# Performance work log

Measured on AMD Instinct MI355X. Metric: run time of the kernel, lower is better.

## Reference

```python
import jax, jax.numpy as jnp
import numpy as np

N = 10000      # n_nodes
T = 8          # input_horizon
P = 2          # prediction_horizon (zeros appended; pred_hor=1 default)
F_IN = 64      # n_features
F_OUT = 64     # n_out_features
H = 128        # h_size
B = 2          # batch
E = 160000     # n_edges
MLPW = 4


def setup_inputs() -> dict:
    key = jax.random.key(0)
    ks = jax.random.split(key, 12)
    s = jnp.float32(0.05)
    return dict(
        x_in=jax.random.normal(ks[0], (B, T, N, F_IN), jnp.float32),
        edge_index=jax.random.randint(ks[1], (2, E), 0, N, jnp.int32),
        edge_weight=jax.random.uniform(ks[2], (E,), jnp.float32),
        gcn_w=jax.random.normal(ks[3], (F_OUT, F_IN), jnp.float32) * s,
        gcn_b=jnp.zeros((F_OUT,), jnp.float32),
        w_ih=jax.random.normal(ks[4], (H, F_OUT), jnp.float32) * s,
        w_hh=jax.random.normal(ks[5], (H, H), jnp.float32) * s,
        b_ih=jnp.zeros((H,), jnp.float32),
        b_hh=jnp.zeros((H,), jnp.float32),
        mlp_w1=jax.random.normal(ks[6], (H * MLPW, H), jnp.float32) * s,
        mlp_b1=jnp.zeros((H * MLPW,), jnp.float32),
        mlp_w2=jax.random.normal(ks[7], (H * MLPW, H * MLPW), jnp.float32) * s,
        mlp_b2=jnp.zeros((H * MLPW,), jnp.float32),
        mlp_w3=jax.random.normal(ks[8], (F_OUT, H * MLPW), jnp.float32) * s,
        mlp_b3=jnp.zeros((F_OUT,), jnp.float32),
    )


def reference(x_in, edge_index, edge_weight, gcn_w, gcn_b,
              w_ih, w_hh, b_ih, b_hh,
              mlp_w1, mlp_b1, mlp_w2, mlp_b2, mlp_w3, mlp_b3):
    Bb = x_in.shape[0]
    x = x_in.reshape(-1, N, F_IN)          # [G, N, F_in], G = B*T
    G = x.shape[0]

    # --- python id-remap (unique -> dense ids); identity when all node ids appear ---
    uv = jnp.unique(edge_index, size=N)
    ei = jnp.searchsorted(uv, edge_index)
    row, col = ei[0], ei[1]

    # --- GCNConv (gcn_norm with add_self_loops=True, fill 1.0) ---
    loop = jnp.arange(N, dtype=row.dtype)
    row_f = jnp.concatenate([row, loop])
    col_f = jnp.concatenate([col, loop])
    ew_f = jnp.concatenate([edge_weight, jnp.ones((N,), edge_weight.dtype)])
    deg = jnp.zeros((N,), edge_weight.dtype).at[col_f].add(ew_f)
    dinv = jnp.where(deg > 0, jax.lax.rsqrt(deg), 0.0)
    norm = dinv[row_f] * ew_f * dinv[col_f]          # [E+N]

    xl = x @ gcn_w.T                                 # [G, N, F_out]
    agg = jnp.zeros((G, N, F_OUT), xl.dtype).at[:, col_f].add(
        xl[:, row_f] * norm[None, :, None])          # scatter-add over targets
    gc = agg + gcn_b                                 # [G, N, F_out]

    # raw row-major view, exactly as torch .view((B*N, T, F_out))
    seq = gc.reshape(Bb * N, T, F_OUT)

    # --- single-layer tanh RNN, batch_first ---
    h0 = jnp.zeros((Bb * N, H), seq.dtype)

    def step(h, xt):
        h = jnp.tanh(xt @ w_ih.T + b_ih + h @ w_hh.T + b_hh)
        return h, h

    _, outs = jax.lax.scan(step, h0, seq.transpose(1, 0, 2))  # [T, B*N, H]
    rnn_out = outs.transpose(1, 0, 2)                          # [B*N, T, H]

    # --- MLP head applied per time step (vectorized) ---
    y = jax.nn.relu(rnn_out @ mlp_w1.T + mlp_b1)
    y = jax.nn.relu(y @ mlp_w2.T + mlp_b2)
    y = y @ mlp_w3.T + mlp_b3                                  # [B*N, T, F_out]

    # prediction slots stay zero (pred_hor=1 default)
    full = jnp.concatenate([y, jnp.zeros((Bb * N, P, F_OUT), y.dtype)], axis=1)
    return full.reshape(Bb, T + P, N, F_OUT)
```

## Files before the change

kernel.cpp:

```cpp
#include <hip/hip_runtime.h>
#include <hip/hip_bf16.h>

#define N_NODES 10000
#define E_EDGES 160000

typedef __attribute__((ext_vector_type(8))) short bf16x8;
typedef __attribute__((ext_vector_type(4))) float f32x4;

__device__ __forceinline__ unsigned short f2b(float f) {
    unsigned int u = __float_as_uint(f);
    u = (u + 0x7fffu + ((u >> 16) & 1u)) >> 16;
    return (unsigned short)u;
}

__device__ __forceinline__ float b2f(unsigned short u) {
    return __uint_as_float(((unsigned int)u) << 16);
}

__device__ __forceinline__ float tanh_fast(float x) {
    float ax = fabsf(x);
    float e = __expf(-2.f * ax);
    float r = (1.f - e) / (1.f + e);
    return copysignf(r, x);
}

__global__ void init_kernel(float* deg, int* cnt) {
    int i = blockIdx.x * 256 + threadIdx.x;
    if (i < N_NODES) { deg[i] = 1.0f; cnt[i] = 0; }
}

__global__ void deg_add_kernel(const int* __restrict__ ei, const float* __restrict__ ew,
                               float* deg, int* cnt) {
    int e = blockIdx.x * 256 + threadIdx.x;
    if (e < E_EDGES) {
        int c = ei[E_EDGES + e];
        atomicAdd(&deg[c], ew[e]);
        atomicAdd(&cnt[c], 1);
    }
}

__global__ void dinv_kernel(const float* __restrict__ deg, float* dinv) {
    int i = blockIdx.x * 256 + threadIdx.x;
    if (i < N_NODES) { float d = deg[i]; dinv[i] = d > 0.f ? rsqrtf(d) : 0.f; }
}

__global__ void scan_kernel(const int* __restrict__ cnt, int* offs, int* cursor) {
    __shared__ int tsum[1024];
    int t = threadIdx.x;
    int base = t * 10;
    int loc[10];
    int s = 0;
    #pragma unroll
    for (int j = 0; j < 10; ++j) {
        int i = base + j;
        int v = (i < N_NODES) ? cnt[i] : 0;
        loc[j] = s; s += v;
    }
    tsum[t] = s;
    __syncthreads();
    for (int d = 1; d < 1024; d <<= 1) {
        int v = (t >= d) ? tsum[t - d] : 0;
        __syncthreads();
        tsum[t] += v;
        __syncthreads();
    }
    int pre = tsum[t] - s;
    #pragma unroll
    for (int j = 0; j < 10; ++j) {
        int i = base + j;
        if (i < N_NODES) { offs[i] = pre + loc[j]; cursor[i] = pre + loc[j]; }
    }
    if (t == 1023) offs[N_NODES] = tsum[1023];
}

__global__ void fill_kernel(const int* __restrict__ ei, const float* __restrict__ ew,
                            const float* __restrict__ dinv, int* cursor,
                            int* erow, float* enorm) {
    int e = blockIdx.x * 256 + threadIdx.x;
    if (e < E_EDGES) {
        int r = ei[e], c = ei[E_EDGES + e];
        float nm = dinv[r] * ew[e] * dinv[c];
        int pos = atomicAdd(&cursor[c], 1);
        erow[pos] = r; enorm[pos] = nm;
    }
}

template<int KS, int K>
__global__ void wconv_kernel(const float* __restrict__ w, unsigned short* __restrict__ o) {
    int idx = blockIdx.x * 256 + threadIdx.x;
    int lane = idx & 63, frag = idx >> 6;
    int nf = frag / KS, ks = frag % KS;
    const float* src = w + (nf * 16 + (lane & 15)) * K + ks * 32 + (lane >> 4) * 8;
    unsigned short* dst = o + frag * 512 + lane * 8;
    float4 v0 = *(const float4*)src;
    float4 v1 = *(const float4*)(src + 4);
    ushort4 h0; h0.x = f2b(v0.x); h0.y = f2b(v0.y); h0.z = f2b(v0.z); h0.w = f2b(v0.w);
    ushort4 h1; h1.x = f2b(v1.x); h1.y = f2b(v1.y); h1.z = f2b(v1.z); h1.w = f2b(v1.w);
    *(ushort4*)dst = h0;
    *(ushort4*)(dst + 4) = h1;
}

__global__ __launch_bounds__(256) void aggregate_kernel(
        const unsigned short* __restrict__ xlt, const int* __restrict__ erow,
        const float* __restrict__ enorm, const int* __restrict__ offs,
        const float* __restrict__ dinv, const float* __restrict__ gcn_b,
        unsigned short* __restrict__ gc) {
    int gwid = (blockIdx.x * 256 + threadIdx.x) >> 6;
    int c = gwid >> 1;
    int gh = (gwid & 1) * 8;
    int lane = threadIdx.x & 63;
    if (c >= N_NODES) return;
    float acc[8];
    float d = dinv[c];
    float wself = d * d;
    const unsigned short* xr = xlt + (long)c * 1024 + gh * 64;
    #pragma unroll
    for (int g = 0; g < 8; ++g) acc[g] = b2f(xr[g * 64 + lane]) * wself;
    int e0 = offs[c], e1 = offs[c + 1];
    for (int e = e0; e < e1; ++e) {
        int r = erow[e];
        float nm = enorm[e];
        const unsigned short* xs = xlt + (long)r * 1024 + gh * 64;
        #pragma unroll
        for (int g = 0; g < 8; ++g) acc[g] += b2f(xs[g * 64 + lane]) * nm;
    }
    float bb = gcn_b[lane];
    #pragma unroll
    for (int g = 0; g < 8; ++g)
        gc[(long)(gh + g) * 640000 + (long)c * 64 + lane] = f2b(acc[g] + bb);
}

template<int NTOT, int BN, int KTOT, bool AF32, int EPI, bool RELU>
__global__ __launch_bounds__(256) void gemm_kernel(
        const void* __restrict__ Aptr, const float* __restrict__ Wp,
        const float* __restrict__ bias0, const float* __restrict__ bias1,
        void* __restrict__ outp) {
    constexpr int WN = BN / 2;
    constexpr int FN = WN / 16;
    __shared__ __align__(16) unsigned short As[128 * 72];
    __shared__ __align__(16) unsigned short Bs[BN * 72];
    const int tid = threadIdx.x;
    const int lane = tid & 63;
    const int wid = tid >> 6;
    const int wm = wid >> 1, wn = wid & 1;
    const long m0 = (long)blockIdx.x * 128;
    const int n0 = blockIdx.y * BN;

    f32x4 acc[4][FN];
    #pragma unroll
    for (int a = 0; a < 4; ++a)
        #pragma unroll
        for (int b = 0; b < FN; ++b)
            acc[a][b] = (f32x4){0.f, 0.f, 0.f, 0.f};

    for (int kt = 0; kt < KTOT / 64; ++kt) {
        if (AF32) {
            const float* Ag = (const float*)Aptr;
            #pragma unroll
            for (int p = 0; p < 8; ++p) {
                int idx = p * 256 + tid;
                int r = idx >> 4, c4 = idx & 15;
                float4 v = *(const float4*)(Ag + (m0 + r) * KTOT + kt * 64 + c4 * 4);
                ushort4 h; h.x = f2b(v.x); h.y = f2b(v.y); h.z = f2b(v.z); h.w = f2b(v.w);
                *(ushort4*)&As[r * 72 + c4 * 4] = h;
            }
        } else {
            const unsigned short* Ag = (const unsigned short*)Aptr;
            #pragma unroll
            for (int p = 0; p < 4; ++p) {
                int idx = p * 256 + tid;
                int r = idx >> 3, c8 = idx & 7;
                *(int4*)&As[r * 72 + c8 * 8] = *(const int4*)(Ag + (m0 + r) * KTOT + kt * 64 + c8 * 8);
            }
        }
        #pragma unroll
        for (int p = 0; p < BN / 16; ++p) {
            int idx = p * 256 + tid;
            int r = idx >> 4, c4 = idx & 15;
            float4 v = *(const float4*)(Wp + (long)(n0 + r) * KTOT + kt * 64 + c4 * 4);
            ushort4 h; h.x = f2b(v.x); h.y = f2b(v.y); h.z = f2b(v.z); h.w = f2b(v.w);
            *(ushort4*)&Bs[r * 72 + c4 * 4] = h;
        }
        __syncthreads();
        #pragma unroll
        for (int ks = 0; ks < 2; ++ks) {
            bf16x8 a[4], b[FN];
            #pragma unroll
            for (int fm = 0; fm < 4; ++fm)
                a[fm] = *(const bf16x8*)&As[(wm * 64 + fm * 16 + (lane & 15)) * 72 + ks * 32 + (lane >> 4) * 8];
            #pragma unroll
            for (int fn = 0; fn < FN; ++fn)
                b[fn] = *(const bf16x8*)&Bs[(wn * WN + fn * 16 + (lane & 15)) * 72 + ks * 32 + (lane >> 4) * 8];
            #pragma unroll
            for (int fm = 0; fm < 4; ++fm)
                #pragma unroll
                for (int fn = 0; fn < FN; ++fn)
                    acc[fm][fn] = __builtin_amdgcn_mfma_f32_16x16x32_bf16(a[fm], b[fn], acc[fm][fn], 0, 0, 0);
        }
        __syncthreads();
    }

    #pragma unroll
    for (int fm = 0; fm < 4; ++fm) {
        #pragma unroll
        for (int fn = 0; fn < FN; ++fn) {
            const int colg = n0 + wn * WN + fn * 16 + (lane & 15);
            float bv = 0.f;
            if (bias0) bv += bias0[colg];
            if (bias1) bv += bias1[colg];
            #pragma unroll
            for (int r = 0; r < 4; ++r) {
                int row = (int)m0 + wm * 64 + fm * 16 + (lane >> 4) * 4 + r;
                float v = acc[fm][fn][r] + bv;
                if (RELU) v = fmaxf(v, 0.f);
                if (EPI == 0) {
                    ((unsigned short*)outp)[(long)(row % N_NODES) * 1024 + (long)(row / N_NODES) * 64 + colg] = f2b(v);
                } else {
                    ((unsigned short*)outp)[(long)row * NTOT + colg] = f2b(v);
                }
            }
        }
    }
}

__global__ __launch_bounds__(256) void rnn_kernel(const unsigned short* __restrict__ xih,
                                                  const float* __restrict__ whh,
                                                  unsigned short* __restrict__ rout) {
    __shared__ __align__(16) unsigned short hs[32 * 128];
    __shared__ __align__(16) unsigned short ws[128 * 128];
    const int tid = threadIdx.x, lane = tid & 63, wid = tid >> 6;
    const long i0 = (long)blockIdx.x * 32;

    #pragma unroll
    for (int p = 0; p < 16; ++p) {
        int idx = p * 256 + tid;
        int n = idx >> 5, k4 = (idx & 31) * 4;
        float4 v = *(const float4*)(whh + n * 128 + k4);
        ushort4 h; h.x = f2b(v.x); h.y = f2b(v.y); h.z = f2b(v.z); h.w = f2b(v.w);
        int byte = (n * 256 + k4 * 2) ^ ((n & 7) << 4);
        *(ushort4*)((char*)ws + byte) = h;
    }
    int4 z = make_int4(0, 0, 0, 0);
    #pragma unroll
    for (int p = 0; p < 2; ++p) ((int4*)hs)[p * 256 + tid] = z;
    __syncthreads();

    unsigned short x2[2][2][2][4];
    #pragma unroll
    for (int fm = 0; fm < 2; ++fm)
        #pragma unroll
        for (int fn = 0; fn < 2; ++fn) {
            int col = wid * 32 + fn * 16 + (lane & 15);
            const unsigned short* src = xih + ((i0 + fm * 16 + (lane >> 4) * 4) * 8 + 0) * 128 + col;
            #pragma unroll
            for (int r = 0; r < 4; ++r) x2[0][fm][fn][r] = src[(long)r * 1024];
        }

    f32x4 acc[2][2];
    #pragma unroll
    for (int t = 0; t < 8; ++t) {
        const int cb = t & 1;
        #pragma unroll
        for (int fm = 0; fm < 2; ++fm)
            #pragma unroll
            for (int fn = 0; fn < 2; ++fn)
                #pragma unroll
                for (int r = 0; r < 4; ++r)
                    acc[fm][fn][r] = b2f(x2[cb][fm][fn][r]);
        if (t < 7) {
            #pragma unroll
            for (int fm = 0; fm < 2; ++fm)
                #pragma unroll
                for (int fn = 0; fn < 2; ++fn) {
                    int col = wid * 32 + fn * 16 + (lane & 15);
                    const unsigned short* src = xih + ((i0 + fm * 16 + (lane >> 4) * 4) * 8 + (t + 1)) * 128 + col;
                    #pragma unroll
                    for (int r = 0; r < 4; ++r) x2[cb ^ 1][fm][fn][r] = src[(long)r * 1024];
                }
        }
        #pragma unroll
        for (int ks = 0; ks < 4; ++ks) {
            bf16x8 a[2], b[2];
            #pragma unroll
            for (int fm = 0; fm < 2; ++fm) {
                int row = fm * 16 + (lane & 15);
                int byte = (row * 256 + ks * 64 + (lane >> 4) * 16) ^ ((row & 7) << 4);
                a[fm] = *(const bf16x8*)((const char*)hs + byte);
            }
            #pragma unroll
            for (int fn = 0; fn < 2; ++fn) {
                int rowb = wid * 32 + fn * 16 + (lane & 15);
                int byte = (rowb * 256 + ks * 64 + (lane >> 4) * 16) ^ ((rowb & 7) << 4);
                b[fn] = *(const bf16x8*)((const char*)ws + byte);
            }
            #pragma unroll
            for (int fm = 0; fm < 2; ++fm)
                #pragma unroll
                for (int fn = 0; fn < 2; ++fn)
                    acc[fm][fn] = __builtin_amdgcn_mfma_f32_16x16x32_bf16(a[fm], b[fn], acc[fm][fn], 0, 0, 0);
        }
        __syncthreads();
        #pragma unroll
        for (int fm = 0; fm < 2; ++fm)
            #pragma unroll
            for (int fn = 0; fn < 2; ++fn) {
                int col = wid * 32 + fn * 16 + (lane & 15);
                #pragma unroll
                for (int r = 0; r < 4; ++r) {
                    int row = fm * 16 + (lane >> 4) * 4 + r;
                    float v = tanh_fast(acc[fm][fn][r]);
                    unsigned short hb = f2b(v);
                    int byte = (row * 256 + col * 2) ^ ((row & 7) << 4);
                    *(unsigned short*)((char*)hs + byte) = hb;
                    rout[((i0 + row) * 8 + t) * 128 + col] = hb;
                }
            }
        __syncthreads();
    }
}

__global__ __launch_bounds__(512) void mlp_kernel(
        const unsigned short* __restrict__ A,
        const unsigned short* __restrict__ w1f, const float* __restrict__ b1,
        const unsigned short* __restrict__ w2f, const float* __restrict__ b2,
        const unsigned short* __restrict__ w3f, const float* __restrict__ b3,
        float* __restrict__ out) {
    __shared__ __align__(16) char smem[81920];
    char* As = smem;
    char* ys = smem + 16384;

    const int tid = threadIdx.x, lane = tid & 63, w = tid >> 6;
    const long r0 = (long)blockIdx.x * 64;

    #pragma unroll
    for (int p = 0; p < 2; ++p) {
        int idx = p * 512 + tid;
        int row = idx >> 4, c16 = idx & 15;
        int4 v = *(const int4*)(A + (r0 + row) * 128 + c16 * 8);
        int byte = (row * 256 + c16 * 16) ^ ((row & 15) << 4);
        *(int4*)(As + byte) = v;
    }
    __syncthreads();

    f32x4 acc[4][4];

    #pragma unroll
    for (int fm = 0; fm < 4; ++fm)
        #pragma unroll
        for (int fn = 0; fn < 4; ++fn) acc[fm][fn] = (f32x4){0.f, 0.f, 0.f, 0.f};
    #pragma unroll
    for (int ks = 0; ks < 4; ++ks) {
        bf16x8 a[4], b[4];
        #pragma unroll
        for (int fm = 0; fm < 4; ++fm) {
            int row = fm * 16 + (lane & 15);
            a[fm] = *(const bf16x8*)(As + ((row * 256 + ks * 64 + (lane >> 4) * 16) ^ ((row & 15) << 4)));
        }
        #pragma unroll
        for (int fn = 0; fn < 4; ++fn)
            b[fn] = *(const bf16x8*)(w1f + (long)((w * 4 + fn) * 4 + ks) * 512 + lane * 8);
        #pragma unroll
        for (int fm = 0; fm < 4; ++fm)
            #pragma unroll
            for (int fn = 0; fn < 4; ++fn)
                acc[fm][fn] = __builtin_amdgcn_mfma_f32_16x16x32_bf16(a[fm], b[fn], acc[fm][fn], 0, 0, 0);
    }
    #pragma unroll
    for (int fn = 0; fn < 4; ++fn) {
        int colg = w * 64 + fn * 16 + (lane & 15);
        float bv = b1[colg];
        #pragma unroll
        for (int fm = 0; fm < 4; ++fm)
            #pragma unroll
            for (int r = 0; r < 4; ++r) {
                int row = fm * 16 + (lane >> 4) * 4 + r;
                float v = fmaxf(acc[fm][fn][r] + bv, 0.f);
                int byte = (row * 1024 + colg * 2) ^ ((row & 15) << 4);
                *(unsigned short*)(ys + byte) = f2b(v);
            }
    }
    __syncthreads();

    #pragma unroll
    for (int fm = 0; fm < 4; ++fm)
        #pragma unroll
        for (int fn = 0; fn < 4; ++fn) acc[fm][fn] = (f32x4){0.f, 0.f, 0.f, 0.f};
    #pragma unroll
    for (int ks = 0; ks < 16; ++ks) {
        bf16x8 a[4], b[4];
        #pragma unroll
        for (int fm = 0; fm < 4; ++fm) {
            int row = fm * 16 + (lane & 15);
            a[fm] = *(const bf16x8*)(ys + ((row * 1024 + ks * 64 + (lane >> 4) * 16) ^ ((row & 15) << 4)));
        }
        #pragma unroll
        for (int fn = 0; fn < 4; ++fn)
            b[fn] = *(const bf16x8*)(w2f + (long)((w * 4 + fn) * 16 + ks) * 512 + lane * 8);
        #pragma unroll
        for (int fm = 0; fm < 4; ++fm)
            #pragma unroll
            for (int fn = 0; fn < 4; ++fn)
                acc[fm][fn] = __builtin_amdgcn_mfma_f32_16x16x32_bf16(a[fm], b[fn], acc[fm][fn], 0, 0, 0);
    }
    __syncthreads();
    #pragma unroll
    for (int fn = 0; fn < 4; ++fn) {
        int colg = w * 64 + fn * 16 + (lane & 15);
        float bv = b2[colg];
        #pragma unroll
        for (int fm = 0; fm < 4; ++fm)
            #pragma unroll
            for (int r = 0; r < 4; ++r) {
                int row = fm * 16 + (lane >> 4) * 4 + r;
                float v = fmaxf(acc[fm][fn][r] + bv, 0.f);
                int byte = (row * 1024 + colg * 2) ^ ((row & 15) << 4);
                *(unsigned short*)(ys + byte) = f2b(v);
            }
    }
    __syncthreads();

    const int fn3 = w & 3, kh = w >> 2;
    f32x4 a3[4];
    #pragma unroll
    for (int fm = 0; fm < 4; ++fm) a3[fm] = (f32x4){0.f, 0.f, 0.f, 0.f};
    #pragma unroll
    for (int ksl = 0; ksl < 8; ++ksl) {
        int ks = kh * 8 + ksl;
        bf16x8 bfrag = *(const bf16x8*)(w3f + (long)(fn3 * 16 + ks) * 512 + lane * 8);
        #pragma unroll
        for (int fm = 0; fm < 4; ++fm) {
            int row = fm * 16 + (lane & 15);
            bf16x8 afrag = *(const bf16x8*)(ys + ((row * 1024 + ks * 64 + (lane >> 4) * 16) ^ ((row & 15) << 4)));
            a3[fm] = __builtin_amdgcn_mfma_f32_16x16x32_bf16(afrag, bfrag, a3[fm], 0, 0, 0);
        }
    }
    __syncthreads();
    if (w >= 4) {
        float* rb = (float*)(ys) + (w - 4) * 1104;
        #pragma unroll
        for (int fm = 0; fm < 4; ++fm)
            #pragma unroll
            for (int r = 0; r < 4; ++r)
                rb[(fm * 16 + (lane >> 4) * 4 + r) * 17 + (lane & 15)] = a3[fm][r];
    }
    __syncthreads();
    if (w < 4) {
        float* rb = (float*)(ys) + w * 1104;
        float bv = b3[fn3 * 16 + (lane & 15)];
        #pragma unroll
        for (int fm = 0; fm < 4; ++fm)
            #pragma unroll
            for (int r = 0; r < 4; ++r) {
                int row = fm * 16 + (lane >> 4) * 4 + r;
                float v = a3[fm][r] + rb[row * 17 + (lane & 15)] + bv;
                long vr = r0 + row;
                out[((vr >> 3) * 10 + (vr & 7)) * 64 + fn3 * 16 + (lane & 15)] = v;
            }
    }
}

extern "C" void kernel_launch(void* const* d_in, const int* in_sizes, int n_in,
                              void* d_out, int out_size, void* d_ws, size_t ws_size,
                              hipStream_t stream) {
    const float* x     = (const float*)d_in[0];
    const int*   ei    = (const int*)  d_in[1];
    const float* ew    = (const float*)d_in[2];
    const float* gcn_w = (const float*)d_in[3];
    const float* gcn_b = (const float*)d_in[4];
    const float* w_ih  = (const float*)d_in[5];
    const float* w_hh  = (const float*)d_in[6];
    const float* b_ih  = (const float*)d_in[7];
    const float* b_hh  = (const float*)d_in[8];
    const float* w1    = (const float*)d_in[9];
    const float* b1    = (const float*)d_in[10];
    const float* w2    = (const float*)d_in[11];
    const float* b2    = (const float*)d_in[12];
    const float* w3    = (const float*)d_in[13];
    const float* b3    = (const float*)d_in[14];

    char* ws = (char*)d_ws;
    unsigned short* xlt  = (unsigned short*)ws;
    unsigned short* rnno = (unsigned short*)ws;
    unsigned short* gc   = (unsigned short*)(ws + 41943040L);
    unsigned short* xih  = (unsigned short*)(ws + 62914560L);
    unsigned short* w1f  = (unsigned short*)(ws + 104857600L);
    unsigned short* w2f  = (unsigned short*)(ws + 104988672L);
    unsigned short* w3f  = (unsigned short*)(ws + 105512960L);
    char* sm = ws + 106954752L;
    float* deg    = (float*)(sm);
    float* dinv   = (float*)(sm + (64 << 10));
    int*   cnt    = (int*)  (sm + (128 << 10));
    int*   offs   = (int*)  (sm + (192 << 10));
    int*   cursor = (int*)  (sm + (256 << 10));
    int*   erow   = (int*)  (sm + (320 << 10));
    float* enorm  = (float*)(sm + (1 << 20));

    hipMemsetAsync(d_out, 0, (size_t)out_size * sizeof(float), stream);

    init_kernel<<<40, 256, 0, stream>>>(deg, cnt);
    deg_add_kernel<<<625, 256, 0, stream>>>(ei, ew, deg, cnt);
    dinv_kernel<<<40, 256, 0, stream>>>(deg, dinv);
    scan_kernel<<<1, 1024, 0, stream>>>(cnt, offs, cursor);
    fill_kernel<<<625, 256, 0, stream>>>(ei, ew, dinv, cursor, erow, enorm);

    wconv_kernel<4, 128><<<32, 256, 0, stream>>>(w1, w1f);
    wconv_kernel<16, 512><<<128, 256, 0, stream>>>(w2, w2f);
    wconv_kernel<16, 512><<<16, 256, 0, stream>>>(w3, w3f);

    gemm_kernel<64, 64, 64, true, 0, false><<<dim3(1250, 1), 256, 0, stream>>>(x, gcn_w, nullptr, nullptr, xlt);
    aggregate_kernel<<<5000, 256, 0, stream>>>(xlt, erow, enorm, offs, dinv, gcn_b, gc);
    gemm_kernel<128, 128, 64, false, 2, false><<<dim3(1250, 1), 256, 0, stream>>>(gc, w_ih, b_ih, b_hh, xih);
    rnn_kernel<<<625, 256, 0, stream>>>(xih, w_hh, rnno);
    mlp_kernel<<<2500, 512, 0, stream>>>(rnno, w1f, b1, w2f, b2, w3f, b3, (float*)d_out);
}
```

Measured before the change: 402.2 us.

## Split MLP hidden dimension into halves to shrink LDS and raise occupancy

Restructures the fused MLP kernel so the 512-wide hidden activations are produced and consumed in two 256-column halves. Layer-1 output for each half feeds a partial K-accumulation of layer 2, and layer-2 output is likewise written and consumed by layer 3 one half at a time. This cuts the shared buffer from 80KB to 48KB and adds a launch-bounds hint for more resident blocks per CU. In exchange it adds extra barriers, and the layer-3 epilogue runs in only half the waves per phase, which may serialize work.

```diff
diff --git a/kernel.cpp b/kernel.cpp
--- a/kernel.cpp
+++ b/kernel.cpp
@@ -319,13 +319,13 @@
     }
 }
 
-__global__ __launch_bounds__(512) void mlp_kernel(
+__global__ __launch_bounds__(512, 4) void mlp_kernel(
         const unsigned short* __restrict__ A,
         const unsigned short* __restrict__ w1f, const float* __restrict__ b1,
         const unsigned short* __restrict__ w2f, const float* __restrict__ b2,
         const unsigned short* __restrict__ w3f, const float* __restrict__ b3,
         float* __restrict__ out) {
-    __shared__ __align__(16) char smem[81920];
+    __shared__ __align__(16) char smem[49152];
     char* As = smem;
     char* ys = smem + 16384;
 
@@ -342,99 +342,99 @@
     }
     __syncthreads();
 
-    f32x4 acc[4][4];
-
+    f32x4 acc2[4][4];
     #pragma unroll
     for (int fm = 0; fm < 4; ++fm)
         #pragma unroll
-        for (int fn = 0; fn < 4; ++fn) acc[fm][fn] = (f32x4){0.f, 0.f, 0.f, 0.f};
-    #pragma unroll
-    for (int ks = 0; ks < 4; ++ks) {
-        bf16x8 a[4], b[4];
-        #pragma unroll
-        for (int fm = 0; fm < 4; ++fm) {
-            int row = fm * 16 + (lane & 15);
-            a[fm] = *(const bf16x8*)(As + ((row * 256 + ks * 64 + (lane >> 4) * 16) ^ ((row & 15) << 4)));
-        }
-        #pragma unroll
-        for (int fn = 0; fn < 4; ++fn)
-            b[fn] = *(const bf16x8*)(w1f + (long)((w * 4 + fn) * 4 + ks) * 512 + lane * 8);
-        #pragma unroll
-        for (int fm = 0; fm < 4; ++fm)
+        for (int fn = 0; fn < 4; ++fn) acc2[fm][fn] = (f32x4){0.f, 0.f, 0.f, 0.f};
+
+    #pragma unroll
+    for (int half = 0; half < 2; ++half) {
+        #pragma unroll
+        for (int fn = 0; fn < 2; ++fn) {
+            f32x4 accy[4];
+            #pragma unroll
+            for (int fm = 0; fm < 4; ++fm) accy[fm] = (f32x4){0.f, 0.f, 0.f, 0.f};
+            #pragma unroll
+            for (int ks = 0; ks < 4; ++ks) {
+                bf16x8 b = *(const bf16x8*)(w1f + (long)((half * 16 + w * 2 + fn) * 4 + ks) * 512 + lane * 8);
+                #pragma unroll
+                for (int fm = 0; fm < 4; ++fm) {
+                    int row = fm * 16 + (lane & 15);
+                    bf16x8 a = *(const bf16x8*)(As + ((row * 256 + ks * 64 + (lane >> 4) * 16) ^ ((row & 15) << 4)));
+                    accy[fm] = __builtin_amdgcn_mfma_f32_16x16x32_bf16(a, b, accy[fm], 0, 0, 0);
+                }
+            }
+            int lcol = w * 32 + fn * 16 + (lane & 15);
+            float bv = b1[half * 256 + lcol];
+            #pragma unroll
+            for (int fm = 0; fm < 4; ++fm)
+                #pragma unroll
+                for (int r = 0; r < 4; ++r) {
+                    int row = fm * 16 + (lane >> 4) * 4 + r;
+                    float v = fmaxf(accy[fm][r] + bv, 0.f);
+                    int byte = (row * 512 + lcol * 2) ^ ((row & 15) << 4);
+                    *(unsigned short*)(ys + byte) = f2b(v);
+                }
+        }
+        __syncthreads();
+        #pragma unroll
+        for (int ks = 0; ks < 8; ++ks) {
+            bf16x8 a[4], b[4];
+            #pragma unroll
+            for (int fm = 0; fm < 4; ++fm) {
+                int row = fm * 16 + (lane & 15);
+                a[fm] = *(const bf16x8*)(ys + ((row * 512 + ks * 64 + (lane >> 4) * 16) ^ ((row & 15) << 4)));
+            }
             #pragma unroll
             for (int fn = 0; fn < 4; ++fn)
-                acc[fm][fn] = __builtin_amdgcn_mfma_f32_16x16x32_bf16(a[fm], b[fn], acc[fm][fn], 0, 0, 0);
-    }
-    #pragma unroll
-    for (int fn = 0; fn < 4; ++fn) {
-        int colg = w * 64 + fn * 16 + (lane & 15);
-        float bv = b1[colg];
-        #pragma unroll
-        for (int fm = 0; fm < 4; ++fm)
-            #pragma unroll
-            for (int r = 0; r < 4; ++r) {
-                int row = fm * 16 + (lane >> 4) * 4 + r;
-                float v = fmaxf(acc[fm][fn][r] + bv, 0.f);
-                int byte = (row * 1024 + colg * 2) ^ ((row & 15) << 4);
-                *(unsigned short*)(ys + byte) = f2b(v);
-            }
-    }
-    __syncthreads();
-
-    #pragma unroll
-    for (int fm = 0; fm < 4; ++fm)
-        #pragma unroll
-        for (int fn = 0; fn < 4; ++fn) acc[fm][fn] = (f32x4){0.f, 0.f, 0.f, 0.f};
-    #pragma unroll
-    for (int ks = 0; ks < 16; ++ks) {
-        bf16x8 a[4], b[4];
-        #pragma unroll
-        for (int fm = 0; fm < 4; ++fm) {
-            int row = fm * 16 + (lane & 15);
-            a[fm] = *(const bf16x8*)(ys + ((row * 1024 + ks * 64 + (lane >> 4) * 16) ^ ((row & 15) << 4)));
-        }
-        #pragma unroll
-        for (int fn = 0; fn < 4; ++fn)
-            b[fn] = *(const bf16x8*)(w2f + (long)((w * 4 + fn) * 16 + ks) * 512 + lane * 8);
-        #pragma unroll
-        for (int fm = 0; fm < 4; ++fm)
-            #pragma unroll
-            for (int fn = 0; fn < 4; ++fn)
-                acc[fm][fn] = __builtin_amdgcn_mfma_f32_16x16x32_bf16(a[fm], b[fn], acc[fm][fn], 0, 0, 0);
-    }
-    __syncthreads();
-    #pragma unroll
-    for (int fn = 0; fn < 4; ++fn) {
-        int colg = w * 64 + fn * 16 + (lane & 15);
-        float bv = b2[colg];
-        #pragma unroll
-        for (int fm = 0; fm < 4; ++fm)
-            #pragma unroll
-            for (int r = 0; r < 4; ++r) {
-                int row = fm * 16 + (lane >> 4) * 4 + r;
-                float v = fmaxf(acc[fm][fn][r] + bv, 0.f);
-                int byte = (row * 1024 + colg * 2) ^ ((row & 15) << 4);
-                *(unsigned short*)(ys + byte) = f2b(v);
-            }
-    }
-    __syncthreads();
-
-    const int fn3 = w & 3, kh = w >> 2;
+                b[fn] = *(const bf16x8*)(w2f + (long)((w * 4 + fn) * 16 + half * 8 + ks) * 512 + lane * 8);
+            #pragma unroll
+            for (int fm = 0; fm < 4; ++fm)
+                #pragma unroll
+                for (int fn = 0; fn < 4; ++fn)
+                    acc2[fm][fn] = __builtin_amdgcn_mfma_f32_16x16x32_bf16(a[fm], b[fn], acc2[fm][fn], 0, 0, 0);
+        }
+        __syncthreads();
+    }
+
+    const int fn3 = w & 3, q = w >> 2;
     f32x4 a3[4];
     #pragma unroll
     for (int fm = 0; fm < 4; ++fm) a3[fm] = (f32x4){0.f, 0.f, 0.f, 0.f};
     #pragma unroll
-    for (int ksl = 0; ksl < 8; ++ksl) {
-        int ks = kh * 8 + ksl;
-        bf16x8 bfrag = *(const bf16x8*)(w3f + (long)(fn3 * 16 + ks) * 512 + lane * 8);
-        #pragma unroll
-        for (int fm = 0; fm < 4; ++fm) {
-            int row = fm * 16 + (lane & 15);
-            bf16x8 afrag = *(const bf16x8*)(ys + ((row * 1024 + ks * 64 + (lane >> 4) * 16) ^ ((row & 15) << 4)));
-            a3[fm] = __builtin_amdgcn_mfma_f32_16x16x32_bf16(afrag, bfrag, a3[fm], 0, 0, 0);
-        }
-    }
-    __syncthreads();
+    for (int half = 0; half < 2; ++half) {
+        if (q == half) {
+            #pragma unroll
+            for (int fn = 0; fn < 4; ++fn) {
+                int lcol = (w & 3) * 64 + fn * 16 + (lane & 15);
+                float bv = b2[w * 64 + fn * 16 + (lane & 15)];
+                #pragma unroll
+                for (int fm = 0; fm < 4; ++fm)
+                    #pragma unroll
+                    for (int r = 0; r < 4; ++r) {
+                        int row = fm * 16 + (lane >> 4) * 4 + r;
+                        float v = fmaxf(acc2[fm][fn][r] + bv, 0.f);
+                        int byte = (row * 512 + lcol * 2) ^ ((row & 15) << 4);
+                        *(unsigned short*)(ys + byte) = f2b(v);
+                    }
+            }
+        }
+        __syncthreads();
+        #pragma unroll
+        for (int ksl = 0; ksl < 4; ++ksl) {
+            int kloc = q * 4 + ksl;
+            bf16x8 b = *(const bf16x8*)(w3f + (long)(fn3 * 16 + half * 8 + kloc) * 512 + lane * 8);
+            #pragma unroll
+            for (int fm = 0; fm < 4; ++fm) {
+                int row = fm * 16 + (lane & 15);
+                bf16x8 a = *(const bf16x8*)(ys + ((row * 512 + kloc * 64 + (lane >> 4) * 16) ^ ((row & 15) << 4)));
+                a3[fm] = __builtin_amdgcn_mfma_f32_16x16x32_bf16(a, b, a3[fm], 0, 0, 0);
+            }
+        }
+        __syncthreads();
+    }
+
     if (w >= 4) {
         float* rb = (float*)(ys) + (w - 4) * 1104;
         #pragma unroll
```

Result: slower. 611.8 us (+52.1%).
